# Optimization experiments

Hardware: AMD Instinct MI355X
Metric: run time of the kernel (lower is better)

The kernel has to match this reference:

```python
import jax, jax.numpy as jnp
import numpy as np

B, S, D = 8, 2048, 1024
LN_EPS = 1e-5
N_EPS = 1e-6


def setup_inputs() -> dict:
    key = jax.random.key(0)
    ks = jax.random.split(key, 6)
    s = 1.0 / np.sqrt(D)
    return {
        "x": jax.random.normal(ks[0], (B, S, D), dtype=jnp.float32),
        "W_w": jax.random.uniform(ks[1], (4 * D, D), jnp.float32, -s, s),
        "W_b": jax.random.uniform(ks[2], (4 * D,), jnp.float32, -s, s),
        "U_w": jax.random.uniform(ks[3], (4 * D, D), jnp.float32, -s, s),
        "gamma": jnp.ones((D,), jnp.float32),
        "beta": jnp.zeros((D,), jnp.float32),
    }


def reference(x, W_w, W_b, U_w, gamma, beta):
    # LayerNorm(x)
    mean = jnp.mean(x, axis=-1, keepdims=True)
    var = jnp.mean(jnp.square(x - mean), axis=-1, keepdims=True)
    h_out = (x - mean) * jax.lax.rsqrt(var + LN_EPS) * gamma + beta

    # Precompute input-side projection for all timesteps: (S, B, 4D)
    xW = jnp.einsum('bsd,ed->sbe', h_out, W_w) + W_b

    def step(carry, xw_t):
        h, c, n = carry
        gates = xw_t + h @ U_w.T  # (B, 4D)
        i, f, o, z = jnp.split(gates, 4, axis=-1)
        i_t = jnp.exp(i)
        f_t = jax.nn.sigmoid(f)
        o_t = jax.nn.sigmoid(o)
        c = f_t * c + i_t * jnp.tanh(z)
        n = f_t * n + i_t
        h = o_t * (c / (n + N_EPS))
        return (h, c, n), h

    h0 = jnp.zeros((B, D), x.dtype)
    c0 = jnp.zeros((B, D), x.dtype)
    n0 = jnp.ones((B, D), x.dtype)
    _, ys = jax.lax.scan(step, (h0, c0, n0), xW)  # ys: (S, B, D)
    y = jnp.transpose(ys, (1, 0, 2))
    return x + y
```

## Files before the change

kernel.cpp:

```cpp
#include <hip/hip_runtime.h>
#include <hip/hip_bf16.h>
#include <hip/hip_cooperative_groups.h>

typedef __attribute__((ext_vector_type(8))) short short8;
typedef __attribute__((ext_vector_type(4))) float f32x4;
typedef __attribute__((ext_vector_type(4))) unsigned int uint4_t;
typedef __attribute__((ext_vector_type(4))) unsigned short ushort4_t;

#define BB 8
#define SS 2048
#define DD 1024
#define EE 4096
#define NB 64

__device__ __forceinline__ unsigned short f2bf(float f) {
  unsigned int u = __builtin_bit_cast(unsigned int, f);
  u += 0x7fffu + ((u >> 16) & 1u);
  return (unsigned short)(u >> 16);
}
__device__ __forceinline__ float bf2f(unsigned short h) {
  unsigned int u = ((unsigned int)h) << 16;
  return __builtin_bit_cast(float, u);
}

__global__ void cvt2_kernel(const float* __restrict__ Wf, const float* __restrict__ Uf,
                            unsigned short* __restrict__ Wb, unsigned short* __restrict__ Ub) {
  const int n4 = EE * DD / 4;
  for (int i = blockIdx.x * blockDim.x + threadIdx.x; i < n4; i += gridDim.x * blockDim.x) {
    float4 w = ((const float4*)Wf)[i];
    float4 u = ((const float4*)Uf)[i];
    ushort4_t wo, uo;
    wo[0] = f2bf(w.x); wo[1] = f2bf(w.y); wo[2] = f2bf(w.z); wo[3] = f2bf(w.w);
    uo[0] = f2bf(u.x); uo[1] = f2bf(u.y); uo[2] = f2bf(u.z); uo[3] = f2bf(u.w);
    ((ushort4_t*)Wb)[i] = wo;
    ((ushort4_t*)Ub)[i] = uo;
  }
}

__global__ void ln_kernel(const float* __restrict__ x, const float* __restrict__ gamma,
                          const float* __restrict__ beta, unsigned short* __restrict__ hout) {
  int row = blockIdx.x;
  int t = threadIdx.x;
  int wid = t >> 6, lane = t & 63;
  float4 v = ((const float4*)(x + (size_t)row * DD))[t];
  float s = v.x + v.y + v.z + v.w;
  float s2 = v.x * v.x + v.y * v.y + v.z * v.z + v.w * v.w;
  for (int o = 32; o; o >>= 1) { s += __shfl_down(s, o); s2 += __shfl_down(s2, o); }
  __shared__ float rs[4], rq[4];
  if (lane == 0) { rs[wid] = s; rq[wid] = s2; }
  __syncthreads();
  float sum = rs[0] + rs[1] + rs[2] + rs[3];
  float sum2 = rq[0] + rq[1] + rq[2] + rq[3];
  float mean = sum * (1.0f / DD);
  float var = sum2 * (1.0f / DD) - mean * mean;
  float rstd = rsqrtf(var + 1e-5f);
  float4 g = ((const float4*)gamma)[t];
  float4 bt = ((const float4*)beta)[t];
  ushort4_t o4;
  o4[0] = f2bf((v.x - mean) * rstd * g.x + bt.x);
  o4[1] = f2bf((v.y - mean) * rstd * g.y + bt.y);
  o4[2] = f2bf((v.z - mean) * rstd * g.z + bt.z);
  o4[3] = f2bf((v.w - mean) * rstd * g.w + bt.w);
  ((ushort4_t*)(hout + (size_t)row * DD))[t] = o4;
}

__launch_bounds__(256)
__global__ void gemm_xw(const unsigned short* __restrict__ A, const unsigned short* __restrict__ Bm,
                        const float* __restrict__ bias, unsigned short* __restrict__ xw) {
  int rowTile = blockIdx.x;
  int colGrp = blockIdx.y;
  int wid = threadIdx.x >> 6;
  int lane = threadIdx.x & 63;
  int colBase = colGrp * 256 + wid * 64;
  int r0 = rowTile * 32 + (lane & 15);
  int kb = (lane >> 4) * 8;
  f32x4 acc[2][4] = {};
  for (int k0 = 0; k0 < DD; k0 += 32) {
    short8 a0 = *(const short8*)(A + (size_t)r0 * DD + k0 + kb);
    short8 a1 = *(const short8*)(A + (size_t)(r0 + 16) * DD + k0 + kb);
#pragma unroll
    for (int c = 0; c < 4; c++) {
      int col = colBase + c * 16 + (lane & 15);
      short8 bf = *(const short8*)(Bm + (size_t)col * DD + k0 + kb);
      acc[0][c] = __builtin_amdgcn_mfma_f32_16x16x32_bf16(a0, bf, acc[0][c], 0, 0, 0);
      acc[1][c] = __builtin_amdgcn_mfma_f32_16x16x32_bf16(a1, bf, acc[1][c], 0, 0, 0);
    }
  }
#pragma unroll
  for (int rr = 0; rr < 2; rr++) {
#pragma unroll
    for (int c = 0; c < 4; c++) {
      int col = colBase + c * 16 + (lane & 15);
      float bv = bias[col];
#pragma unroll
      for (int r2 = 0; r2 < 4; r2++) {
        int R = rowTile * 32 + rr * 16 + (lane >> 4) * 4 + r2;
        int b = R >> 11, sIdx = R & 2047;
        xw[(size_t)sIdx * (BB * EE) + (size_t)b * EE + col] = f2bf(acc[rr][c][r2] + bv);
      }
    }
  }
}

__launch_bounds__(256, 1)
__global__ void scan_kernel(const unsigned short* __restrict__ xw, const unsigned short* __restrict__ Ub,
                            const float* __restrict__ x, float* __restrict__ out,
                            unsigned short* __restrict__ hbuf, int* __restrict__ flags) {
  int bl = blockIdx.x;
  int tid = threadIdx.x;
  int wid = tid >> 6, lane = tid & 63;
  int d0 = bl * 16;

  __shared__ __align__(16) unsigned short h_lds[8 * 1024];
  __shared__ float g_lds[4][8][16];
  __shared__ char pad_lds[80 * 1024];
  ((volatile char*)pad_lds)[tid] = 0;

  int ecol = wid * 1024 + d0 + (lane & 15);
  int kb = (lane >> 4) * 8;
  short8 u[32];
#pragma unroll
  for (int kk = 0; kk < 32; kk++)
    u[kk] = *(const short8*)(Ub + (size_t)ecol * DD + kk * 32 + kb);
#pragma unroll
  for (int kk = 0; kk < 32; kk++)
    asm volatile("" : "+v"(u[kk]));

  float c_s = 0.0f, n_s = 1.0f;
  int ub = tid >> 4, ud = tid & 15;
  bool upd = tid < BB * 16;
  int arow = lane & 7;
  int bq = (lane >> 4) * 4;

  for (int s = 0; s < SS; s++) {
    const unsigned short* xwp = xw + (size_t)s * (BB * EE) + (size_t)wid * 1024 + d0 + (lane & 15);
    unsigned short xv[4] = {0, 0, 0, 0};
    if (bq < BB) {
#pragma unroll
      for (int r2 = 0; r2 < 4; r2++) xv[r2] = xwp[(size_t)(bq + r2) * EE];
    }
    float xin = 0.0f;
    size_t oi = 0;
    if (upd) {
      oi = (size_t)ub * (SS * DD) + (size_t)s * DD + d0 + ud;
      xin = x[oi];
    }

    if (s != 0) {
      int f = __hip_atomic_load(flags + lane * 32, __ATOMIC_RELAXED, __HIP_MEMORY_SCOPE_AGENT);
      while (__any(f < s)) {
        f = __hip_atomic_load(flags + lane * 32, __ATOMIC_RELAXED, __HIP_MEMORY_SCOPE_AGENT);
      }
    }

    {
      const unsigned int* hg = (const unsigned int*)(hbuf + (size_t)(s & 1) * (BB * DD));
      unsigned int tmp[16];
#pragma unroll
      for (int i = 0; i < 16; i++)
        tmp[i] = __hip_atomic_load(hg + tid + i * 256, __ATOMIC_RELAXED, __HIP_MEMORY_SCOPE_AGENT);
#pragma unroll
      for (int i = 0; i < 16; i++) {
        int dw = tid + i * 256;
        int row = dw >> 9;
        int byte = (row * 2048 + (dw & 511) * 4) ^ (row << 4);
        *(unsigned int*)((char*)h_lds + byte) = tmp[i];
      }
    }
    __syncthreads();

    f32x4 a0 = {}, a1 = {}, a2 = {}, a3 = {};
#pragma unroll
    for (int kk = 0; kk < 32; kk += 4) {
      int base = arow * 2048 + (kk * 32 + kb) * 2;
      short8 f0 = *(const short8*)((char*)h_lds + ((base) ^ (arow << 4)));
      short8 f1 = *(const short8*)((char*)h_lds + ((base + 64) ^ (arow << 4)));
      short8 f2 = *(const short8*)((char*)h_lds + ((base + 128) ^ (arow << 4)));
      short8 f3 = *(const short8*)((char*)h_lds + ((base + 192) ^ (arow << 4)));
      a0 = __builtin_amdgcn_mfma_f32_16x16x32_bf16(f0, u[kk], a0, 0, 0, 0);
      a1 = __builtin_amdgcn_mfma_f32_16x16x32_bf16(f1, u[kk + 1], a1, 0, 0, 0);
      a2 = __builtin_amdgcn_mfma_f32_16x16x32_bf16(f2, u[kk + 2], a2, 0, 0, 0);
      a3 = __builtin_amdgcn_mfma_f32_16x16x32_bf16(f3, u[kk + 3], a3, 0, 0, 0);
    }
    f32x4 acc = (a0 + a1) + (a2 + a3);

    if (bq < BB) {
#pragma unroll
      for (int r2 = 0; r2 < 4; r2++)
        g_lds[wid][bq + r2][lane & 15] = acc[r2] + bf2f(xv[r2]);
    }
    __syncthreads();

    float h_val = 0.0f;
    if (upd) {
      float gi = g_lds[0][ub][ud], gf = g_lds[1][ub][ud];
      float go = g_lds[2][ub][ud], gz = g_lds[3][ub][ud];
      float it = __expf(gi);
      float ft = 1.0f / (1.0f + __expf(-gf));
      float ot = 1.0f / (1.0f + __expf(-go));
      float az = fabsf(gz);
      float e2 = __expf(2.0f * az);
      float zt = __builtin_copysignf(1.0f - 2.0f / (e2 + 1.0f), gz);
      c_s = ft * c_s + it * zt;
      n_s = ft * n_s + it;
      h_val = ot * (c_s / (n_s + 1e-6f));
      __hip_atomic_store(hbuf + (size_t)((s + 1) & 1) * (BB * DD) + ub * DD + d0 + ud,
                         f2bf(h_val), __ATOMIC_RELAXED, __HIP_MEMORY_SCOPE_AGENT);
      asm volatile("s_waitcnt vmcnt(0)" ::: "memory");
    }
    __syncthreads();
    if (tid == 0)
      __hip_atomic_store(flags + bl * 32, s + 1, __ATOMIC_RELAXED, __HIP_MEMORY_SCOPE_AGENT);
    if (upd)
      __builtin_nontemporal_store(xin + h_val, out + oi);
  }
}

extern "C" void kernel_launch(void* const* d_in, const int* in_sizes, int n_in,
                              void* d_out, int out_size, void* d_ws, size_t ws_size,
                              hipStream_t stream) {
  const float* xp = (const float*)d_in[0];
  const float* Wwf = (const float*)d_in[1];
  const float* Wbias = (const float*)d_in[2];
  const float* Uwf = (const float*)d_in[3];
  const float* gamma = (const float*)d_in[4];
  const float* beta = (const float*)d_in[5];
  float* outp = (float*)d_out;

  char* w = (char*)d_ws;
  unsigned short* Wb = (unsigned short*)(w);
  unsigned short* Ub = (unsigned short*)(w + 8388608);
  unsigned short* hout = (unsigned short*)(w + 16777216);
  unsigned short* xw = (unsigned short*)(w + 50331648);
  unsigned short* hbuf = (unsigned short*)(w + 184549376);
  int* flags = (int*)(w + 184549376 + 32768);

  hipMemsetAsync((void*)hbuf, 0, 32768 + 8192, stream);

  hipLaunchKernelGGL(cvt2_kernel, dim3(1024), dim3(256), 0, stream, Wwf, Uwf, Wb, Ub);
  hipLaunchKernelGGL(ln_kernel, dim3(BB * SS), dim3(256), 0, stream, xp, gamma, beta, hout);
  hipLaunchKernelGGL(gemm_xw, dim3(512, 16), dim3(256), 0, stream, hout, Wb, Wbias, xw);

  void* args[6];
  const unsigned short* xw_c = xw;
  const unsigned short* ub_c = Ub;
  args[0] = (void*)&xw_c;
  args[1] = (void*)&ub_c;
  args[2] = (void*)&xp;
  args[3] = (void*)&outp;
  args[4] = (void*)&hbuf;
  args[5] = (void*)&flags;
  hipLaunchCooperativeKernel((void*)scan_kernel, dim3(NB), dim3(256), args, 0, stream);
}
```

Before: 5.866 ms.

## Pack gate update into one wave, drop per-step barrier, enlarge GEMM row tile

```diff
diff --git a/kernel.cpp b/kernel.cpp
--- a/kernel.cpp
+++ b/kernel.cpp
@@ -4,6 +4,7 @@
 
 typedef __attribute__((ext_vector_type(8))) short short8;
 typedef __attribute__((ext_vector_type(4))) float f32x4;
+typedef __attribute__((ext_vector_type(2))) float f32x2;
 typedef __attribute__((ext_vector_type(4))) unsigned int uint4_t;
 typedef __attribute__((ext_vector_type(4))) unsigned short ushort4_t;
 
@@ -72,29 +73,32 @@
   int wid = threadIdx.x >> 6;
   int lane = threadIdx.x & 63;
   int colBase = colGrp * 256 + wid * 64;
-  int r0 = rowTile * 32 + (lane & 15);
+  int r0 = rowTile * 64 + (lane & 15);
   int kb = (lane >> 4) * 8;
-  f32x4 acc[2][4] = {};
+  f32x4 acc[4][4] = {};
   for (int k0 = 0; k0 < DD; k0 += 32) {
-    short8 a0 = *(const short8*)(A + (size_t)r0 * DD + k0 + kb);
-    short8 a1 = *(const short8*)(A + (size_t)(r0 + 16) * DD + k0 + kb);
+    short8 af[4];
+#pragma unroll
+    for (int rr = 0; rr < 4; rr++)
+      af[rr] = *(const short8*)(A + (size_t)(r0 + rr * 16) * DD + k0 + kb);
 #pragma unroll
     for (int c = 0; c < 4; c++) {
       int col = colBase + c * 16 + (lane & 15);
       short8 bf = *(const short8*)(Bm + (size_t)col * DD + k0 + kb);
-      acc[0][c] = __builtin_amdgcn_mfma_f32_16x16x32_bf16(a0, bf, acc[0][c], 0, 0, 0);
-      acc[1][c] = __builtin_amdgcn_mfma_f32_16x16x32_bf16(a1, bf, acc[1][c], 0, 0, 0);
-    }
-  }
-#pragma unroll
-  for (int rr = 0; rr < 2; rr++) {
+#pragma unroll
+      for (int rr = 0; rr < 4; rr++)
+        acc[rr][c] = __builtin_amdgcn_mfma_f32_16x16x32_bf16(af[rr], bf, acc[rr][c], 0, 0, 0);
+    }
+  }
+#pragma unroll
+  for (int rr = 0; rr < 4; rr++) {
 #pragma unroll
     for (int c = 0; c < 4; c++) {
       int col = colBase + c * 16 + (lane & 15);
       float bv = bias[col];
 #pragma unroll
       for (int r2 = 0; r2 < 4; r2++) {
-        int R = rowTile * 32 + rr * 16 + (lane >> 4) * 4 + r2;
+        int R = rowTile * 64 + rr * 16 + (lane >> 4) * 4 + r2;
         int b = R >> 11, sIdx = R & 2047;
         xw[(size_t)sIdx * (BB * EE) + (size_t)b * EE + col] = f2bf(acc[rr][c][r2] + bv);
       }
@@ -126,9 +130,9 @@
   for (int kk = 0; kk < 32; kk++)
     asm volatile("" : "+v"(u[kk]));
 
-  float c_s = 0.0f, n_s = 1.0f;
-  int ub = tid >> 4, ud = tid & 15;
-  bool upd = tid < BB * 16;
+  f32x2 c_s = {0.f, 0.f}, n_s = {1.f, 1.f};
+  int ub8 = tid >> 3, ud2 = (tid & 7) * 2;
+  bool upd = tid < 64;
   int arow = lane & 7;
   int bq = (lane >> 4) * 4;
 
@@ -139,11 +143,11 @@
 #pragma unroll
       for (int r2 = 0; r2 < 4; r2++) xv[r2] = xwp[(size_t)(bq + r2) * EE];
     }
-    float xin = 0.0f;
+    f32x2 xin = {0.f, 0.f};
     size_t oi = 0;
     if (upd) {
-      oi = (size_t)ub * (SS * DD) + (size_t)s * DD + d0 + ud;
-      xin = x[oi];
+      oi = (size_t)ub8 * (SS * DD) + (size_t)s * DD + d0 + ud2;
+      xin = *(const f32x2*)(x + oi);
     }
 
     if (s != 0) {
@@ -191,28 +195,32 @@
     }
     __syncthreads();
 
-    float h_val = 0.0f;
     if (upd) {
-      float gi = g_lds[0][ub][ud], gf = g_lds[1][ub][ud];
-      float go = g_lds[2][ub][ud], gz = g_lds[3][ub][ud];
-      float it = __expf(gi);
-      float ft = 1.0f / (1.0f + __expf(-gf));
-      float ot = 1.0f / (1.0f + __expf(-go));
-      float az = fabsf(gz);
-      float e2 = __expf(2.0f * az);
-      float zt = __builtin_copysignf(1.0f - 2.0f / (e2 + 1.0f), gz);
-      c_s = ft * c_s + it * zt;
-      n_s = ft * n_s + it;
-      h_val = ot * (c_s / (n_s + 1e-6f));
-      __hip_atomic_store(hbuf + (size_t)((s + 1) & 1) * (BB * DD) + ub * DD + d0 + ud,
-                         f2bf(h_val), __ATOMIC_RELAXED, __HIP_MEMORY_SCOPE_AGENT);
+      f32x2 gi = *(const f32x2*)&g_lds[0][ub8][ud2];
+      f32x2 gf = *(const f32x2*)&g_lds[1][ub8][ud2];
+      f32x2 go = *(const f32x2*)&g_lds[2][ub8][ud2];
+      f32x2 gz = *(const f32x2*)&g_lds[3][ub8][ud2];
+      float it0 = __expf(gi.x), it1 = __expf(gi.y);
+      float ft0 = 1.f / (1.f + __expf(-gf.x)), ft1 = 1.f / (1.f + __expf(-gf.y));
+      float ot0 = 1.f / (1.f + __expf(-go.x)), ot1 = 1.f / (1.f + __expf(-go.y));
+      float az0 = fabsf(gz.x), az1 = fabsf(gz.y);
+      float e20 = __expf(2.f * az0), e21 = __expf(2.f * az1);
+      float zt0 = __builtin_copysignf(1.f - 2.f / (e20 + 1.f), gz.x);
+      float zt1 = __builtin_copysignf(1.f - 2.f / (e21 + 1.f), gz.y);
+      c_s.x = ft0 * c_s.x + it0 * zt0;  c_s.y = ft1 * c_s.y + it1 * zt1;
+      n_s.x = ft0 * n_s.x + it0;        n_s.y = ft1 * n_s.y + it1;
+      float h0 = ot0 * (c_s.x / (n_s.x + 1e-6f));
+      float h1 = ot1 * (c_s.y / (n_s.y + 1e-6f));
+      unsigned int hp2 = ((unsigned int)f2bf(h1) << 16) | (unsigned int)f2bf(h0);
+      unsigned int* hw = (unsigned int*)hbuf + (size_t)((s + 1) & 1) * 4096 +
+                         ub8 * 512 + (d0 >> 1) + (tid & 7);
+      __hip_atomic_store(hw, hp2, __ATOMIC_RELAXED, __HIP_MEMORY_SCOPE_AGENT);
       asm volatile("s_waitcnt vmcnt(0)" ::: "memory");
-    }
-    __syncthreads();
-    if (tid == 0)
-      __hip_atomic_store(flags + bl * 32, s + 1, __ATOMIC_RELAXED, __HIP_MEMORY_SCOPE_AGENT);
-    if (upd)
-      __builtin_nontemporal_store(xin + h_val, out + oi);
+      if (tid == 0)
+        __hip_atomic_store(flags + bl * 32, s + 1, __ATOMIC_RELAXED, __HIP_MEMORY_SCOPE_AGENT);
+      __builtin_nontemporal_store(xin.x + h0, out + oi);
+      __builtin_nontemporal_store(xin.y + h1, out + oi + 1);
+    }
   }
 }
 
@@ -239,7 +247,7 @@
 
   hipLaunchKernelGGL(cvt2_kernel, dim3(1024), dim3(256), 0, stream, Wwf, Uwf, Wb, Ub);
   hipLaunchKernelGGL(ln_kernel, dim3(BB * SS), dim3(256), 0, stream, xp, gamma, beta, hout);
-  hipLaunchKernelGGL(gemm_xw, dim3(512, 16), dim3(256), 0, stream, hout, Wb, Wbias, xw);
+  hipLaunchKernelGGL(gemm_xw, dim3(256, 16), dim3(256), 0, stream, hout, Wb, Wbias, xw);
 
   void* args[6];
   const unsigned short* xw_c = xw;
```

Result: slower. 6.040 ms (+3.0%).

## Poll flags from one wave, widen h loads, and enlarge GEMM row tile

Applied to the files above, without the earlier changes.

```diff
diff --git a/kernel.cpp b/kernel.cpp
--- a/kernel.cpp
+++ b/kernel.cpp
@@ -4,8 +4,8 @@
 
 typedef __attribute__((ext_vector_type(8))) short short8;
 typedef __attribute__((ext_vector_type(4))) float f32x4;
-typedef __attribute__((ext_vector_type(4))) unsigned int uint4_t;
 typedef __attribute__((ext_vector_type(4))) unsigned short ushort4_t;
+typedef unsigned long long u64;
 
 #define BB 8
 #define SS 2048
@@ -72,29 +72,32 @@
   int wid = threadIdx.x >> 6;
   int lane = threadIdx.x & 63;
   int colBase = colGrp * 256 + wid * 64;
-  int r0 = rowTile * 32 + (lane & 15);
+  int r0 = rowTile * 64 + (lane & 15);
   int kb = (lane >> 4) * 8;
-  f32x4 acc[2][4] = {};
+  f32x4 acc[4][4] = {};
   for (int k0 = 0; k0 < DD; k0 += 32) {
-    short8 a0 = *(const short8*)(A + (size_t)r0 * DD + k0 + kb);
-    short8 a1 = *(const short8*)(A + (size_t)(r0 + 16) * DD + k0 + kb);
+    short8 af[4];
+#pragma unroll
+    for (int rr = 0; rr < 4; rr++)
+      af[rr] = *(const short8*)(A + (size_t)(r0 + rr * 16) * DD + k0 + kb);
 #pragma unroll
     for (int c = 0; c < 4; c++) {
       int col = colBase + c * 16 + (lane & 15);
       short8 bf = *(const short8*)(Bm + (size_t)col * DD + k0 + kb);
-      acc[0][c] = __builtin_amdgcn_mfma_f32_16x16x32_bf16(a0, bf, acc[0][c], 0, 0, 0);
-      acc[1][c] = __builtin_amdgcn_mfma_f32_16x16x32_bf16(a1, bf, acc[1][c], 0, 0, 0);
-    }
-  }
-#pragma unroll
-  for (int rr = 0; rr < 2; rr++) {
+#pragma unroll
+      for (int rr = 0; rr < 4; rr++)
+        acc[rr][c] = __builtin_amdgcn_mfma_f32_16x16x32_bf16(af[rr], bf, acc[rr][c], 0, 0, 0);
+    }
+  }
+#pragma unroll
+  for (int rr = 0; rr < 4; rr++) {
 #pragma unroll
     for (int c = 0; c < 4; c++) {
       int col = colBase + c * 16 + (lane & 15);
       float bv = bias[col];
 #pragma unroll
       for (int r2 = 0; r2 < 4; r2++) {
-        int R = rowTile * 32 + rr * 16 + (lane >> 4) * 4 + r2;
+        int R = rowTile * 64 + rr * 16 + (lane >> 4) * 4 + r2;
         int b = R >> 11, sIdx = R & 2047;
         xw[(size_t)sIdx * (BB * EE) + (size_t)b * EE + col] = f2bf(acc[rr][c][r2] + bv);
       }
@@ -113,8 +116,10 @@
 
   __shared__ __align__(16) unsigned short h_lds[8 * 1024];
   __shared__ float g_lds[4][8][16];
+  __shared__ int ready;
   __shared__ char pad_lds[80 * 1024];
   ((volatile char*)pad_lds)[tid] = 0;
+  if (tid == 0) ready = -1;
 
   int ecol = wid * 1024 + d0 + (lane & 15);
   int kb = (lane >> 4) * 8;
@@ -132,6 +137,8 @@
   int arow = lane & 7;
   int bq = (lane >> 4) * 4;
 
+  __syncthreads();
+
   for (int s = 0; s < SS; s++) {
     const unsigned short* xwp = xw + (size_t)s * (BB * EE) + (size_t)wid * 1024 + d0 + (lane & 15);
     unsigned short xv[4] = {0, 0, 0, 0};
@@ -147,24 +154,29 @@
     }
 
     if (s != 0) {
-      int f = __hip_atomic_load(flags + lane * 32, __ATOMIC_RELAXED, __HIP_MEMORY_SCOPE_AGENT);
-      while (__any(f < s)) {
-        f = __hip_atomic_load(flags + lane * 32, __ATOMIC_RELAXED, __HIP_MEMORY_SCOPE_AGENT);
+      if (wid == 0) {
+        int f = __hip_atomic_load(flags + lane * 32, __ATOMIC_RELAXED, __HIP_MEMORY_SCOPE_AGENT);
+        while (__any(f < s)) {
+          f = __hip_atomic_load(flags + lane * 32, __ATOMIC_RELAXED, __HIP_MEMORY_SCOPE_AGENT);
+        }
+        __hip_atomic_store(&ready, s, __ATOMIC_RELEASE, __HIP_MEMORY_SCOPE_WORKGROUP);
+      } else {
+        while (__hip_atomic_load(&ready, __ATOMIC_ACQUIRE, __HIP_MEMORY_SCOPE_WORKGROUP) < s) {}
       }
     }
 
     {
-      const unsigned int* hg = (const unsigned int*)(hbuf + (size_t)(s & 1) * (BB * DD));
-      unsigned int tmp[16];
-#pragma unroll
-      for (int i = 0; i < 16; i++)
+      const u64* hg = (const u64*)(hbuf + (size_t)(s & 1) * (BB * DD));
+      u64 tmp[8];
+#pragma unroll
+      for (int i = 0; i < 8; i++)
         tmp[i] = __hip_atomic_load(hg + tid + i * 256, __ATOMIC_RELAXED, __HIP_MEMORY_SCOPE_AGENT);
 #pragma unroll
-      for (int i = 0; i < 16; i++) {
-        int dw = tid + i * 256;
-        int row = dw >> 9;
-        int byte = (row * 2048 + (dw & 511) * 4) ^ (row << 4);
-        *(unsigned int*)((char*)h_lds + byte) = tmp[i];
+      for (int i = 0; i < 8; i++) {
+        int q = tid + i * 256;
+        int row = q >> 8, qoff = q & 255;
+        int byte = (row * 2048 + qoff * 8) ^ (row << 4);
+        *(u64*)((char*)h_lds + byte) = tmp[i];
       }
     }
     __syncthreads();
@@ -239,7 +251,7 @@
 
   hipLaunchKernelGGL(cvt2_kernel, dim3(1024), dim3(256), 0, stream, Wwf, Uwf, Wb, Ub);
   hipLaunchKernelGGL(ln_kernel, dim3(BB * SS), dim3(256), 0, stream, xp, gamma, beta, hout);
-  hipLaunchKernelGGL(gemm_xw, dim3(512, 16), dim3(256), 0, stream, hout, Wb, Wbias, xw);
+  hipLaunchKernelGGL(gemm_xw, dim3(256, 16), dim3(256), 0, stream, hout, Wb, Wbias, xw);
 
   void* args[6];
   const unsigned short* xw_c = xw;
```

After: 5.755 ms. No clear change (-1.9%).
